# Optimization experiments

Hardware: AMD Instinct MI355X
Metric: run time of the kernel (lower is better)

The kernel has to match this reference:

```python
import jax, jax.numpy as jnp
import numpy as np

H = 512   # hidden_size
L = 20    # num_labels
B, S = 32, 256


def _uniform(key, shape, k):
    return jax.random.uniform(key, shape, minval=-k, maxval=k, dtype=jnp.float32)


def setup_inputs() -> dict:
    key = jax.random.key(0)
    ks = iter(jax.random.split(key, 40))
    k = 1.0 / np.sqrt(H)
    inp = {
        "inputs": jax.random.normal(next(ks), (B, S, H), dtype=jnp.float32),
        "labels": jax.random.randint(next(ks), (B, S), 0, L),
        "mask": jnp.ones((B, S), dtype=jnp.int32),
    }
    for layer, din in ((0, H), (1, 2 * H)):
        for d in ("f", "b"):
            inp[f"w_ih_l{layer}{d}"] = _uniform(next(ks), (4 * H, din), k)
            inp[f"w_hh_l{layer}{d}"] = _uniform(next(ks), (4 * H, H), k)
            inp[f"b_ih_l{layer}{d}"] = _uniform(next(ks), (4 * H,), k)
            inp[f"b_hh_l{layer}{d}"] = _uniform(next(ks), (4 * H,), k)
    kf = 1.0 / np.sqrt(2 * H)
    inp["fc_w"] = _uniform(next(ks), (L, 2 * H), kf)
    inp["fc_b"] = _uniform(next(ks), (L,), kf)
    inp["trans_m"] = jax.random.normal(next(ks), (L, L), dtype=jnp.float32) * 0.1
    inp["start_scores"] = jax.random.normal(next(ks), (L,), dtype=jnp.float32) * 0.1
    inp["end_scores"] = jax.random.normal(next(ks), (L,), dtype=jnp.float32) * 0.1
    return inp


def _lstm_dir(x, wih, whh, bih, bhh, reverse):
    # x: [S, B, Din] -> hs: [S, B, H] (outputs in original time order)
    _, b, _ = x.shape
    hh = whh.shape[1]
    xw = jnp.einsum('sbd,gd->sbg', x, wih) + bih + bhh  # precompute input projections

    def step(carry, xt):
        h, c = carry
        g = xt + h @ whh.T  # [B, 4H]
        i, f, gg, o = jnp.split(g, 4, axis=-1)  # pytorch gate order i,f,g,o
        c = jax.nn.sigmoid(f) * c + jax.nn.sigmoid(i) * jnp.tanh(gg)
        h = jax.nn.sigmoid(o) * jnp.tanh(c)
        return (h, c), h

    init = (jnp.zeros((b, hh), x.dtype), jnp.zeros((b, hh), x.dtype))
    _, hs = jax.lax.scan(step, init, xw, reverse=reverse)
    return hs


def _crf_loss(logits, tags, maskf, trans, start, end):
    # logits [S,B,L], tags [S,B], maskf [S,B] float. Returns per-sample NLL [B].
    s, b, n = logits.shape
    # --- normalizer (forward algorithm) ---
    alpha0 = logits[0] + start  # [B, n]

    def step(alpha, inp):
        emit, m = inp  # emit [B,n], m [B]
        tmp = alpha[:, :, None] + trans[None, :, :] + emit[:, None, :]  # [B, from, to]
        new = jax.nn.logsumexp(tmp, axis=1)
        alpha = jnp.where(m[:, None] > 0, new, alpha)
        return alpha, None

    alpha, _ = jax.lax.scan(step, alpha0, (logits[1:], maskf[1:]))
    norm = jax.nn.logsumexp(alpha + end, axis=1)  # [B]
    # --- gold path score ---
    emit = jnp.take_along_axis(logits, tags[:, :, None], axis=2)[:, :, 0] * maskf  # [S,B]
    trans_sc = trans[tags[:-1], tags[1:]] * maskf[1:]  # [S-1,B]
    last_idx = maskf.sum(0).astype(jnp.int32) - 1  # [B]
    last_tags = tags[last_idx, jnp.arange(b)]
    gold = emit.sum(0) + trans_sc.sum(0) + start[tags[0]] + end[last_tags]
    return norm - gold


def reference(inputs, labels, mask,
              w_ih_l0f, w_hh_l0f, b_ih_l0f, b_hh_l0f,
              w_ih_l0b, w_hh_l0b, b_ih_l0b, b_hh_l0b,
              w_ih_l1f, w_hh_l1f, b_ih_l1f, b_hh_l1f,
              w_ih_l1b, w_hh_l1b, b_ih_l1b, b_hh_l1b,
              fc_w, fc_b, trans_m, start_scores, end_scores):
    x = jnp.transpose(inputs, (1, 0, 2))  # [S,B,H]
    h0 = jnp.concatenate([
        _lstm_dir(x, w_ih_l0f, w_hh_l0f, b_ih_l0f, b_hh_l0f, False),
        _lstm_dir(x, w_ih_l0b, w_hh_l0b, b_ih_l0b, b_hh_l0b, True),
    ], axis=-1)  # [S,B,2H]
    h1 = jnp.concatenate([
        _lstm_dir(h0, w_ih_l1f, w_hh_l1f, b_ih_l1f, b_hh_l1f, False),
        _lstm_dir(h0, w_ih_l1b, w_hh_l1b, b_ih_l1b, b_hh_l1b, True),
    ], axis=-1)  # [S,B,2H]
    logits = h1 @ fc_w.T + fc_b  # [S,B,L]
    tags = labels.T  # [S,B]
    maskf = mask.T.astype(logits.dtype)
    loss = _crf_loss(logits, tags, maskf, trans_m, start_scores, end_scores)
    return loss.mean()
```

## Files before the change

### kernel.cpp

```cpp
#include <hip/hip_runtime.h>

#define Sx 256
#define Bx 32
#define Hx 512
#define Gx 2048
#define Lx 20
#define Rx 8192

typedef __attribute__((ext_vector_type(8))) short short8;
typedef __attribute__((ext_vector_type(4))) float f32x4;
typedef __attribute__((ext_vector_type(16))) float f32x16;

__device__ __forceinline__ unsigned short f2bf(float f) {
  union { float f; unsigned u; } v; v.f = f;
  unsigned u = v.u;
  return (unsigned short)((u + 0x7fffu + ((u >> 16) & 1u)) >> 16);
}
__device__ __forceinline__ float bf2f(unsigned short h) {
  union { unsigned u; float f; } v; v.u = ((unsigned)h) << 16;
  return v.f;
}
__device__ __forceinline__ float bfh(unsigned long long x, int r) {
  return bf2f((unsigned short)((x >> (16 * r)) & 0xffffull));
}

__device__ __forceinline__ float fsigm(float x) {
  return __builtin_amdgcn_rcpf(1.0f + __builtin_amdgcn_exp2f(-1.44269504f * x));
}
__device__ __forceinline__ float ftanh(float x) {
  return __builtin_fmaf(-2.0f,
      __builtin_amdgcn_rcpf(1.0f + __builtin_amdgcn_exp2f(2.88539008f * x)), 1.0f);
}
#define L2E 1.44269504088896f
#define LN2 0.69314718055995f

#define GLD16(gp, lp) __builtin_amdgcn_global_load_lds( \
    (const __attribute__((address_space(1))) void*)(gp), \
    (__attribute__((address_space(3))) void*)(lp), 16, 0, 0)


__global__ void k_pack_x(const float* __restrict__ x, unsigned short* __restrict__ xbf) {
  int tid = blockIdx.x * 256 + threadIdx.x;
  int h = tid & (Hx - 1);
  int r = tid >> 9;
  int b = r & 31;
  int t = r >> 5;
  xbf[tid] = f2bf(x[(b * Sx + t) * Hx + h]);
}

__global__ __launch_bounds__(256) void k_prep(
    const float* __restrict__ s0, const float* __restrict__ s1,
    const float* __restrict__ s2, const float* __restrict__ s3,
    const float* __restrict__ s4, const float* __restrict__ s5,
    const float* __restrict__ s6, const float* __restrict__ s7,
    unsigned short* __restrict__ d0, unsigned short* __restrict__ d1,
    unsigned short* __restrict__ d2, unsigned short* __restrict__ d3,
    unsigned short* __restrict__ d4, unsigned short* __restrict__ d5,
    unsigned short* __restrict__ d6, unsigned short* __restrict__ d7,
    const float* __restrict__ ba0, const float* __restrict__ bb0, float* __restrict__ bo0,
    const float* __restrict__ ba1, const float* __restrict__ bb1, float* __restrict__ bo1,
    const float* __restrict__ ba2, const float* __restrict__ bb2, float* __restrict__ bo2,
    const float* __restrict__ ba3, const float* __restrict__ bb3, float* __restrict__ bo3)
{
  const int blk = blockIdx.x;
  const int tid = threadIdx.x;
  if (blk < 5120) {
    const float* srcs[8] = { s0, s1, s2, s3, s4, s5, s6, s7 };
    unsigned short* dsts[8] = { d0, d1, d2, d3, d4, d5, d6, d7 };
    size_t e0 = ((size_t)blk * 256 + tid) * 8;
    int m = (int)(e0 >> 20);
    int seg; size_t base;
    if (m < 4)      { seg = m; base = (size_t)m << 20; }
    else if (m < 6) { seg = 4; base = (size_t)4 << 20; }
    else if (m < 8) { seg = 5; base = (size_t)6 << 20; }
    else if (m == 8){ seg = 6; base = (size_t)8 << 20; }
    else            { seg = 7; base = (size_t)9 << 20; }
    size_t off = e0 - base;
    f32x4 a = *(const f32x4*)(srcs[seg] + off);
    f32x4 b = *(const f32x4*)(srcs[seg] + off + 4);
    short8 o;
    o[0] = (short)f2bf(a[0]); o[1] = (short)f2bf(a[1]);
    o[2] = (short)f2bf(a[2]); o[3] = (short)f2bf(a[3]);
    o[4] = (short)f2bf(b[0]); o[5] = (short)f2bf(b[1]);
    o[6] = (short)f2bf(b[2]); o[7] = (short)f2bf(b[3]);
    *(short8*)(dsts[seg] + off) = o;
  } else {
    int j = blk - 5120;
    const float* bas[4] = { ba0, ba1, ba2, ba3 };
    const float* bbs[4] = { bb0, bb1, bb2, bb3 };
    float* bos[4] = { bo0, bo1, bo2, bo3 };
    int i0 = tid * 8;
    f32x4 x0 = *(const f32x4*)(bas[j] + i0);
    f32x4 x1 = *(const f32x4*)(bas[j] + i0 + 4);
    f32x4 y0 = *(const f32x4*)(bbs[j] + i0);
    f32x4 y1 = *(const f32x4*)(bbs[j] + i0 + 4);
    *(f32x4*)(bos[j] + i0) = x0 + y0;
    *(f32x4*)(bos[j] + i0 + 4) = x1 + y1;
  }
}

__global__ __launch_bounds__(256) void k_gemm(
    const unsigned short* __restrict__ A,
    const unsigned short* __restrict__ Bw,
    const float* __restrict__ bias,
    unsigned short* __restrict__ C,
    int M, int N, int K)
{
  const int bn = blockIdx.x, bm = blockIdx.y;
  const int tid = threadIdx.x;
  const int w = tid >> 6, lane = tid & 63;
  const int wr = w >> 1, wc = w & 1;
  const int lo = lane & 15, qd = lane >> 4;

  __shared__ unsigned short As[128 * 64];
  __shared__ unsigned short Bs[128 * 64];

  f32x4 acc[4][4] = {};

  const int cis = (lane & 7) ^ (lane >> 3);
  const int ktn = K >> 6;
  for (int kt = 0; kt < ktn; ++kt) {
    __syncthreads();
#pragma unroll
    for (int p = 0; p < 4; ++p) {
      int rowb = w * 8 + p * 32;
      int row = rowb + (lane >> 3);
      GLD16(&A[(size_t)(bm * 128 + row) * K + kt * 64 + cis * 8], &As[rowb * 64]);
      GLD16(&Bw[(size_t)(bn * 128 + row) * K + kt * 64 + cis * 8], &Bs[rowb * 64]);
    }
    __syncthreads();
#pragma unroll
    for (int kk = 0; kk < 2; ++kk) {
      short8 af[4], bfr[4];
#pragma unroll
      for (int mi = 0; mi < 4; ++mi)
        af[mi] = *(const short8*)&As[(wr * 64 + mi * 16 + lo) * 64
                                     + (((kk * 4 + qd) ^ (lo & 7)) * 8)];
#pragma unroll
      for (int ni = 0; ni < 4; ++ni)
        bfr[ni] = *(const short8*)&Bs[(wc * 64 + ni * 16 + lo) * 64
                                      + (((kk * 4 + qd) ^ (lo & 7)) * 8)];
#pragma unroll
      for (int mi = 0; mi < 4; ++mi)
#pragma unroll
        for (int ni = 0; ni < 4; ++ni)
          acc[mi][ni] = __builtin_amdgcn_mfma_f32_16x16x32_bf16(af[mi], bfr[ni], acc[mi][ni], 0, 0, 0);
    }
  }
#pragma unroll
  for (int mi = 0; mi < 4; ++mi) {
#pragma unroll
    for (int ni = 0; ni < 4; ++ni) {
      int n = bn * 128 + wc * 64 + ni * 16 + lo;
      float bv = bias[n];
      int wsb = (n >> 4) & 31, cg = n >> 9, jl = n & 15;
      size_t base = (size_t)wsb * (Rx * 64) + (size_t)cg * 16 + jl;
#pragma unroll
      for (int r = 0; r < 4; ++r) {
        int m = bm * 128 + wr * 64 + mi * 16 + qd * 4 + r;
        C[base + (size_t)m * 64] = f2bf(acc[mi][ni][r] + bv);
      }
    }
  }
}

__global__ __launch_bounds__(256) void k_gemm_t(
    const unsigned short* __restrict__ hT,
    const unsigned short* __restrict__ Bw,
    const float* __restrict__ bias,
    unsigned short* __restrict__ C,
    int M, int N, int K)
{
  const int bn = blockIdx.x, bm = blockIdx.y;
  const int tid = threadIdx.x;
  const int w = tid >> 6, lane = tid & 63;
  const int wr = w >> 1, wc = w & 1;
  const int lo = lane & 15, qd = lane >> 4;

  __shared__ unsigned short As[128 * 64];
  __shared__ unsigned short Bs[128 * 64];

  f32x4 acc[4][4] = {};

  const int cis = (lane & 7) ^ (lane >> 3);
  const int ktn = K >> 6;
  for (int kt = 0; kt < ktn; ++kt) {
    __syncthreads();
#pragma unroll
    for (int p = 0; p < 4; ++p) {
      int rowb = w * 8 + p * 32;
      int row = rowb + (lane >> 3);
      int grow = bm * 128 + row;
      int t = grow >> 5, b = grow & 31;
      int k = kt * 64 + cis * 8;
      int dirx = k >> 9, kk2 = k & 511;
      GLD16(&hT[(size_t)dirx * (Sx * 16384) + (size_t)t * 16384
                + (size_t)(kk2 >> 3) * 256 + b * 8], &As[rowb * 64]);
      GLD16(&Bw[(size_t)(bn * 128 + row) * K + kt * 64 + cis * 8], &Bs[rowb * 64]);
    }
    __syncthreads();
#pragma unroll
    for (int kk = 0; kk < 2; ++kk) {
      short8 af[4], bfr[4];
#pragma unroll
      for (int mi = 0; mi < 4; ++mi)
        af[mi] = *(const short8*)&As[(wr * 64 + mi * 16 + lo) * 64
                                     + (((kk * 4 + qd) ^ (lo & 7)) * 8)];
#pragma unroll
      for (int ni = 0; ni < 4; ++ni)
        bfr[ni] = *(const short8*)&Bs[(wc * 64 + ni * 16 + lo) * 64
                                      + (((kk * 4 + qd) ^ (lo & 7)) * 8)];
#pragma unroll
      for (int mi = 0; mi < 4; ++mi)
#pragma unroll
        for (int ni = 0; ni < 4; ++ni)
          acc[mi][ni] = __builtin_amdgcn_mfma_f32_16x16x32_bf16(af[mi], bfr[ni], acc[mi][ni], 0, 0, 0);
    }
  }
#pragma unroll
  for (int mi = 0; mi < 4; ++mi) {
#pragma unroll
    for (int ni = 0; ni < 4; ++ni) {
      int n = bn * 128 + wc * 64 + ni * 16 + lo;
      float bv = bias[n];
      int wsb = (n >> 4) & 31, cg = n >> 9, jl = n & 15;
      size_t base = (size_t)wsb * (Rx * 64) + (size_t)cg * 16 + jl;
#pragma unroll
      for (int r = 0; r < 4; ++r) {
        int m = bm * 128 + wr * 64 + mi * 16 + qd * 4 + r;
        C[base + (size_t)m * 64] = f2bf(acc[mi][ni][r] + bv);
      }
    }
  }
}

__global__ __launch_bounds__(256, 1) void k_lstm(
    const unsigned short* __restrict__ xwF,
    const unsigned short* __restrict__ xwB,
    const unsigned short* __restrict__ whF,
    const unsigned short* __restrict__ whB,
    unsigned short* __restrict__ hT,
    unsigned int* __restrict__ flags,
    unsigned int* __restrict__ done)
{
  const int wg = blockIdx.x;
  const int tid = threadIdx.x;

  __shared__ unsigned short Ws[64 * 512];

  if (wg >= 64) {
    asm volatile("s_setprio 0");
    float a = 1.0f + (float)tid, bm = 1.0000001f, cm = 1.0e-7f;
    for (;;) {
#pragma unroll 8
      for (int i = 0; i < 512; ++i) a = __builtin_fmaf(a, bm, cm);
      if (__hip_atomic_load(done, __ATOMIC_RELAXED, __HIP_MEMORY_SCOPE_AGENT) >= 64u) break;
    }
    if (a == 123.456789f) ((volatile float*)hT)[0] = a;
    return;
  }

  asm volatile("s_setprio 3");
  const int dir = wg >> 5;
  const int vs = wg & 31;
  const int j0 = vs * 16;
  const unsigned short* xw = (dir ? xwB : xwF) + (size_t)vs * (Rx * 64);
  const unsigned short* wh = dir ? whB : whF;
  unsigned short* hTd = hT + (size_t)dir * (Sx * 16384);
  unsigned int* fl = flags + dir * 32 * 32;

  {
    const int l6 = tid & 63;
#pragma unroll
    for (int i = 0; i < 16; ++i) {
      int rr = (tid >> 6) * 16 + i;
      int g = ((rr >> 4) << 9) + j0 + (rr & 15);
      int pc = l6 ^ (rr & 7);
      *(short8*)&Ws[rr * 512 + pc * 8] = *(const short8*)&wh[(size_t)g * Hx + l6 * 8];
    }
  }
  __syncthreads();
  if (tid >= 64) return;

  const int lane = tid;
  const int bn = lane & 31;
  const int q  = lane >> 5;

  float cst[2][4] = {};

  for (int s = 0; s < Sx; ++s) {
    const int t = dir ? (Sx - 1 - s) : s;

    const unsigned short* xwt = xw + ((size_t)t * 32 + bn) * 64 + q * 4;
    unsigned long long xg[4][2];
#pragma unroll
    for (int c = 0; c < 4; ++c)
#pragma unroll
      for (int jg = 0; jg < 2; ++jg)
        xg[c][jg] = *(const unsigned long long*)(xwt + c * 16 + jg * 8);
    __asm__ __volatile__("" ::: "memory");

    f32x16 acc0, acc1;

    if (s > 0) {
      const unsigned tgt = (unsigned)s;
      const int tp = dir ? (t + 1) : (t - 1);
      const unsigned short* hb = hTd + (size_t)tp * 16384 + lane * 8;

      short8 hreg[32];
      for (;;) {
        unsigned v = __hip_atomic_load(fl + (lane & 31) * 32,
                                       __ATOMIC_RELAXED, __HIP_MEMORY_SCOPE_AGENT);
#pragma unroll
        for (int ks = 0; ks < 32; ++ks)
          hreg[ks] = *(const short8*)(hb + ks * 512);
#pragma unroll
        for (int ks = 0; ks < 32; ++ks)
          asm volatile("" :: "v"(hreg[ks]));
        if (__all((int)(v >= tgt))) break;
        __asm__ __volatile__("" ::: "memory");
      }
      __builtin_amdgcn_sched_barrier(0);

      f32x16 a0 = {}, a1 = {}, b0 = {}, b1 = {};
#pragma unroll
      for (int ks = 0; ks < 32; ks += 2) {
        int lc0 = ks * 2 + q, lc1 = (ks + 1) * 2 + q;
        int pc0 = lc0 ^ (bn & 7), pc1 = lc1 ^ (bn & 7);
        short8 af00 = *(const short8*)&Ws[bn * 512 + pc0 * 8];
        short8 af10 = *(const short8*)&Ws[(32 + bn) * 512 + pc0 * 8];
        short8 af01 = *(const short8*)&Ws[bn * 512 + pc1 * 8];
        short8 af11 = *(const short8*)&Ws[(32 + bn) * 512 + pc1 * 8];
        a0 = __builtin_amdgcn_mfma_f32_32x32x16_bf16(af00, hreg[ks],     a0, 0, 0, 0);
        a1 = __builtin_amdgcn_mfma_f32_32x32x16_bf16(af10, hreg[ks],     a1, 0, 0, 0);
        b0 = __builtin_amdgcn_mfma_f32_32x32x16_bf16(af01, hreg[ks + 1], b0, 0, 0, 0);
        b1 = __builtin_amdgcn_mfma_f32_32x32x16_bf16(af11, hreg[ks + 1], b1, 0, 0, 0);
      }
      acc0 = a0 + b0;
      acc1 = a1 + b1;
    } else {
      acc0 = (f32x16){};
      acc1 = (f32x16){};
    }

#pragma unroll
    for (int jg = 0; jg < 2; ++jg) {
      unsigned long long hv = 0;
#pragma unroll
      for (int r = 0; r < 4; ++r) {
        float iv = acc0[jg * 4 + r]     + bfh(xg[0][jg], r);
        float fv = acc0[8 + jg * 4 + r] + bfh(xg[1][jg], r);
        float gv = acc1[jg * 4 + r]     + bfh(xg[2][jg], r);
        float ov = acc1[8 + jg * 4 + r] + bfh(xg[3][jg], r);
        float ct = fsigm(fv) * cst[jg][r] + fsigm(iv) * ftanh(gv);
        cst[jg][r] = ct;
        float hvf = fsigm(ov) * ftanh(ct);
        hv |= (unsigned long long)f2bf(hvf) << (16 * r);
      }
      unsigned short* hw = hTd + (size_t)t * 16384 + ((size_t)(vs * 2 + jg) * 32 + bn) * 8 + q * 4;
      __hip_atomic_store((unsigned long long*)hw, hv,
                         __ATOMIC_RELAXED, __HIP_MEMORY_SCOPE_AGENT);
    }

    __asm__ __volatile__("s_waitcnt vmcnt(0)" ::: "memory");
    if (lane == 0)
      __hip_atomic_store(fl + vs * 32, (unsigned)(s + 1),
                         __ATOMIC_RELAXED, __HIP_MEMORY_SCOPE_AGENT);
  }

  if (lane == 0)
    __hip_atomic_fetch_add(done, 1u, __ATOMIC_RELAXED, __HIP_MEMORY_SCOPE_AGENT);
}

__global__ __launch_bounds__(256) void k_fc(
    const unsigned short* __restrict__ h1T,
    const float* __restrict__ fcw,
    const float* __restrict__ fcb,
    float* __restrict__ logits)
{
  int row = blockIdx.x;
  int t = row >> 5, b = row & 31;
  int l = threadIdx.x & 31;
  int sl = threadIdx.x >> 5;
  __shared__ float red[8][32];
  float p = 0.f;
  if (l < Lx) {
#pragma unroll 4
    for (int kt = sl * 16; kt < sl * 16 + 16; ++kt) {
      int k = kt * 8;
      int dir = k >> 9, kk = k & 511;
      const unsigned short* hp = h1T + (size_t)dir * (Sx * 16384) + (size_t)t * 16384
                                 + ((size_t)(kk >> 3) * 32 + b) * 8;
      short8 hv = *(const short8*)hp;
      const float* wr = fcw + l * 1024 + k;
      f32x4 w0 = *(const f32x4*)wr;
      f32x4 w1 = *(const f32x4*)(wr + 4);
      p += bf2f((unsigned short)hv[0]) * w0[0] + bf2f((unsigned short)hv[1]) * w0[1]
         + bf2f((unsigned short)hv[2]) * w0[2] + bf2f((unsigned short)hv[3]) * w0[3]
         + bf2f((unsigned short)hv[4]) * w1[0] + bf2f((unsigned short)hv[5]) * w1[1]
         + bf2f((unsigned short)hv[6]) * w1[2] + bf2f((unsigned short)hv[7]) * w1[3];
    }
  }
  red[sl][l] = p;
  __syncthreads();
  if (threadIdx.x < Lx) {
    float s = fcb[threadIdx.x];
#pragma unroll
    for (int i = 0; i < 8; ++i) s += red[i][threadIdx.x];
    logits[(size_t)row * Lx + threadIdx.x] = s;
  }
}

__global__ __launch_bounds__(64) void k_crf(
    const float* __restrict__ logits,
    const int* __restrict__ labels,
    const int* __restrict__ mask,
    const float* __restrict__ trans,
    const float* __restrict__ startv,
    const float* __restrict__ endv,
    float* __restrict__ out)
{
  int b = blockIdx.x;
  int tid = threadIdx.x;
  __shared__ float tr[Lx * Lx];
  __shared__ float al[2][Lx];
  __shared__ float norm_s;
  for (int i = tid; i < Lx * Lx; i += 64) tr[i] = trans[i];
  if (tid < Lx) al[0][tid] = logits[b * Lx + tid] + startv[tid];
  __syncthreads();
  int cur = 0;
  float em = (tid < Lx) ? logits[((size_t)1 * Bx + b) * Lx + tid] : 0.f;
  int m = mask[b * Sx + 1];
  for (int t = 1; t < Sx; ++t) {
    float em_next = 0.f;
    int m_next = 0;
    if (t + 1 < Sx) {
      if (tid < Lx) em_next = logits[((size_t)(t + 1) * Bx + b) * Lx + tid];
      m_next = mask[b * Sx + t + 1];
    }
    if (tid < Lx) {
      int to = tid;
      float v[Lx];
      float mx = -1e30f;
#pragma unroll
      for (int f = 0; f < Lx; ++f) { v[f] = al[cur][f] + tr[f * Lx + to]; mx = fmaxf(mx, v[f]); }
      float sum = 0.f;
#pragma unroll
      for (int f = 0; f < Lx; ++f) sum += __builtin_amdgcn_exp2f((v[f] - mx) * L2E);
      float nv = mx + LN2 * __builtin_amdgcn_logf(sum) + em;
      al[1 - cur][to] = (m > 0) ? nv : al[cur][to];
    }
    __syncthreads();
    cur ^= 1;
    em = em_next;
    m = m_next;
  }
  if (tid == 0) {
    float mx = -1e30f;
    for (int l = 0; l < Lx; ++l) mx = fmaxf(mx, al[cur][l] + endv[l]);
    float s = 0.f;
    for (int l = 0; l < Lx; ++l) s += __builtin_amdgcn_exp2f((al[cur][l] + endv[l] - mx) * L2E);
    norm_s = mx + LN2 * __builtin_amdgcn_logf(s);
  }
  __syncthreads();
  const int* lab = labels + b * Sx;
  const int* msk = mask + b * Sx;
  float part = 0.f;
  int msum = 0;
  for (int t = tid; t < Sx; t += 64) {
    int mm = msk[t];
    int tg = lab[t];
    if (mm > 0) {
      part += logits[((size_t)t * Bx + b) * Lx + tg];
      if (t >= 1) part += tr[lab[t - 1] * Lx + tg];
      msum++;
    }
  }
#pragma unroll
  for (int o = 32; o > 0; o >>= 1) {
    part += __shfl_down(part, o, 64);
    msum += __shfl_down(msum, o, 64);
  }
  if (tid == 0) {
    float gold = part + startv[lab[0]] + endv[lab[msum - 1]];
    atomicAdd(out, (norm_s - gold) * (1.0f / 32.0f));
  }
}


extern "C" void kernel_launch(void* const* d_in, const int* in_sizes, int n_in,
                              void* d_out, int out_size, void* d_ws, size_t ws_size,
                              hipStream_t stream)
{
  const float* x      = (const float*)d_in[0];
  const int* labels   = (const int*)d_in[1];
  const int* mask     = (const int*)d_in[2];
  const float* wih0f  = (const float*)d_in[3];
  const float* whh0f  = (const float*)d_in[4];
  const float* bih0f  = (const float*)d_in[5];
  const float* bhh0f  = (const float*)d_in[6];
  const float* wih0b  = (const float*)d_in[7];
  const float* whh0b  = (const float*)d_in[8];
  const float* bih0b  = (const float*)d_in[9];
  const float* bhh0b  = (const float*)d_in[10];
  const float* wih1f  = (const float*)d_in[11];
  const float* whh1f  = (const float*)d_in[12];
  const float* bih1f  = (const float*)d_in[13];
  const float* bhh1f  = (const float*)d_in[14];
  const float* wih1b  = (const float*)d_in[15];
  const float* whh1b  = (const float*)d_in[16];
  const float* bih1b  = (const float*)d_in[17];
  const float* bhh1b  = (const float*)d_in[18];
  const float* fcw    = (const float*)d_in[19];
  const float* fcb    = (const float*)d_in[20];
  const float* transm = (const float*)d_in[21];
  const float* startv = (const float*)d_in[22];
  const float* endv   = (const float*)d_in[23];

  char* p = (char*)d_ws;
  auto alloc = [&](size_t bytes) -> char* {
    char* r = p;
    p += (bytes + 255) & ~((size_t)255);
    return r;
  };

  unsigned short* x_bf    = (unsigned short*)alloc((size_t)Rx * Hx * 2);
  unsigned short* wih0f_b = (unsigned short*)alloc((size_t)Gx * Hx * 2);
  unsigned short* wih0b_b = (unsigned short*)alloc((size_t)Gx * Hx * 2);
  unsigned short* whh0f_b = (unsigned short*)alloc((size_t)Gx * Hx * 2);
  unsigned short* whh0b_b = (unsigned short*)alloc((size_t)Gx * Hx * 2);
  unsigned short* wih1f_b = (unsigned short*)alloc((size_t)Gx * 1024 * 2);
  unsigned short* wih1b_b = (unsigned short*)alloc((size_t)Gx * 1024 * 2);
  unsigned short* whh1f_b = (unsigned short*)alloc((size_t)Gx * Hx * 2);
  unsigned short* whh1b_b = (unsigned short*)alloc((size_t)Gx * Hx * 2);
  float* bias0f = (float*)alloc(Gx * 4);
  float* bias0b = (float*)alloc(Gx * 4);
  float* bias1f = (float*)alloc(Gx * 4);
  float* bias1b = (float*)alloc(Gx * 4);
  unsigned short* xw_f = (unsigned short*)alloc((size_t)Rx * Gx * 2);
  unsigned short* xw_b = (unsigned short*)alloc((size_t)Rx * Gx * 2);
  unsigned short* h0T  = (unsigned short*)alloc((size_t)2 * Sx * 16384 * 2);
  unsigned short* h1T  = (unsigned short*)alloc((size_t)2 * Sx * 16384 * 2);
  float* logits = (float*)alloc((size_t)Rx * Lx * 4);
  unsigned int* flagsA = (unsigned int*)alloc(2 * 32 * 32 * 4);
  unsigned int* flagsB = (unsigned int*)alloc(2 * 32 * 32 * 4);
  unsigned int* doneA  = (unsigned int*)alloc(256);
  unsigned int* doneB  = (unsigned int*)alloc(256);

  if ((size_t)(p - (char*)d_ws) > ws_size) return;

  hipMemsetAsync(flagsA, 0, 2 * 32 * 32 * 4, stream);
  hipMemsetAsync(flagsB, 0, 2 * 32 * 32 * 4, stream);
  hipMemsetAsync(doneA, 0, 256, stream);
  hipMemsetAsync(doneB, 0, 256, stream);

  k_pack_x<<<(Rx * Hx) / 256, 256, 0, stream>>>(x, x_bf);
  k_prep<<<5124, 256, 0, stream>>>(
      wih0f, wih0b, whh0f, whh0b, wih1f, wih1b, whh1f, whh1b,
      wih0f_b, wih0b_b, whh0f_b, whh0b_b, wih1f_b, wih1b_b, whh1f_b, whh1b_b,
      bih0f, bhh0f, bias0f,
      bih0b, bhh0b, bias0b,
      bih1f, bhh1f, bias1f,
      bih1b, bhh1b, bias1b);

  k_gemm<<<dim3(Gx / 128, Rx / 128), 256, 0, stream>>>(x_bf, wih0f_b, bias0f, xw_f, Rx, Gx, Hx);
  k_gemm<<<dim3(Gx / 128, Rx / 128), 256, 0, stream>>>(x_bf, wih0b_b, bias0b, xw_b, Rx, Gx, Hx);
  k_lstm<<<256, 256, 0, stream>>>(xw_f, xw_b, whh0f_b, whh0b_b, h0T, flagsA, doneA);

  k_gemm_t<<<dim3(Gx / 128, Rx / 128), 256, 0, stream>>>(h0T, wih1f_b, bias1f, xw_f, Rx, Gx, 1024);
  k_gemm_t<<<dim3(Gx / 128, Rx / 128), 256, 0, stream>>>(h0T, wih1b_b, bias1b, xw_b, Rx, Gx, 1024);
  k_lstm<<<256, 256, 0, stream>>>(xw_f, xw_b, whh1f_b, whh1b_b, h1T, flagsB, doneB);

  k_fc<<<Rx, 256, 0, stream>>>(h1T, fcw, fcb, logits);
  hipMemsetAsync(d_out, 0, 4, stream);
  k_crf<<<Bx, 64, 0, stream>>>(logits, labels, mask, transm, startv, endv, (float*)d_out);
}
```

Measured before the change: 2.502 ms.

## Overlap layer-1 input projection GEMM with layer-0 LSTM recurrence using idle workgroups

Workgroups that previously only spun in the layer-0 LSTM kernel now pull GEMM tiles from an atomic work queue. Each tile waits on the per-direction timestep flags until the h0 rows it needs are ready, then computes the layer-1 input projection into new buffers. The goal is to hide the separate layer-1 GEMM launches behind the serial recurrence. Tiles are ordered from the middle outward so they become ready early for both directions. In exchange it adds two extra xw buffers and possible contention (memory bandwidth, flag polling) with the latency-critical recurrent workgroups.

```diff
diff --git a/kernel.cpp b/kernel.cpp
--- a/kernel.cpp
+++ b/kernel.cpp
@@ -164,76 +164,6 @@
   }
 }
 
-__global__ __launch_bounds__(256) void k_gemm_t(
-    const unsigned short* __restrict__ hT,
-    const unsigned short* __restrict__ Bw,
-    const float* __restrict__ bias,
-    unsigned short* __restrict__ C,
-    int M, int N, int K)
-{
-  const int bn = blockIdx.x, bm = blockIdx.y;
-  const int tid = threadIdx.x;
-  const int w = tid >> 6, lane = tid & 63;
-  const int wr = w >> 1, wc = w & 1;
-  const int lo = lane & 15, qd = lane >> 4;
-
-  __shared__ unsigned short As[128 * 64];
-  __shared__ unsigned short Bs[128 * 64];
-
-  f32x4 acc[4][4] = {};
-
-  const int cis = (lane & 7) ^ (lane >> 3);
-  const int ktn = K >> 6;
-  for (int kt = 0; kt < ktn; ++kt) {
-    __syncthreads();
-#pragma unroll
-    for (int p = 0; p < 4; ++p) {
-      int rowb = w * 8 + p * 32;
-      int row = rowb + (lane >> 3);
-      int grow = bm * 128 + row;
-      int t = grow >> 5, b = grow & 31;
-      int k = kt * 64 + cis * 8;
-      int dirx = k >> 9, kk2 = k & 511;
-      GLD16(&hT[(size_t)dirx * (Sx * 16384) + (size_t)t * 16384
-                + (size_t)(kk2 >> 3) * 256 + b * 8], &As[rowb * 64]);
-      GLD16(&Bw[(size_t)(bn * 128 + row) * K + kt * 64 + cis * 8], &Bs[rowb * 64]);
-    }
-    __syncthreads();
-#pragma unroll
-    for (int kk = 0; kk < 2; ++kk) {
-      short8 af[4], bfr[4];
-#pragma unroll
-      for (int mi = 0; mi < 4; ++mi)
-        af[mi] = *(const short8*)&As[(wr * 64 + mi * 16 + lo) * 64
-                                     + (((kk * 4 + qd) ^ (lo & 7)) * 8)];
-#pragma unroll
-      for (int ni = 0; ni < 4; ++ni)
-        bfr[ni] = *(const short8*)&Bs[(wc * 64 + ni * 16 + lo) * 64
-                                      + (((kk * 4 + qd) ^ (lo & 7)) * 8)];
-#pragma unroll
-      for (int mi = 0; mi < 4; ++mi)
-#pragma unroll
-        for (int ni = 0; ni < 4; ++ni)
-          acc[mi][ni] = __builtin_amdgcn_mfma_f32_16x16x32_bf16(af[mi], bfr[ni], acc[mi][ni], 0, 0, 0);
-    }
-  }
-#pragma unroll
-  for (int mi = 0; mi < 4; ++mi) {
-#pragma unroll
-    for (int ni = 0; ni < 4; ++ni) {
-      int n = bn * 128 + wc * 64 + ni * 16 + lo;
-      float bv = bias[n];
-      int wsb = (n >> 4) & 31, cg = n >> 9, jl = n & 15;
-      size_t base = (size_t)wsb * (Rx * 64) + (size_t)cg * 16 + jl;
-#pragma unroll
-      for (int r = 0; r < 4; ++r) {
-        int m = bm * 128 + wr * 64 + mi * 16 + qd * 4 + r;
-        C[base + (size_t)m * 64] = f2bf(acc[mi][ni][r] + bv);
-      }
-    }
-  }
-}
-
 __global__ __launch_bounds__(256, 1) void k_lstm(
     const unsigned short* __restrict__ xwF,
     const unsigned short* __restrict__ xwB,
@@ -241,22 +171,119 @@
     const unsigned short* __restrict__ whB,
     unsigned short* __restrict__ hT,
     unsigned int* __restrict__ flags,
-    unsigned int* __restrict__ done)
+    unsigned int* __restrict__ done,
+    const unsigned short* __restrict__ gWf,
+    const unsigned short* __restrict__ gWb,
+    const float* __restrict__ gBf,
+    const float* __restrict__ gBb,
+    unsigned short* __restrict__ gCf,
+    unsigned short* __restrict__ gCb,
+    unsigned int* __restrict__ wq,
+    int gw)
 {
   const int wg = blockIdx.x;
   const int tid = threadIdx.x;
 
   __shared__ unsigned short Ws[64 * 512];
+  __shared__ unsigned widx;
 
   if (wg >= 64) {
     asm volatile("s_setprio 0");
-    float a = 1.0f + (float)tid, bm = 1.0000001f, cm = 1.0e-7f;
-    for (;;) {
+    if (gw) {
+      const int w = tid >> 6, lane = tid & 63;
+      const int wr = w >> 1, wc = w & 1;
+      const int lo = lane & 15, qd = lane >> 4;
+      const int cis = (lane & 7) ^ (lane >> 3);
+      for (;;) {
+        if (tid == 0) widx = atomicAdd(wq, 1u);
+        __syncthreads();
+        unsigned idx = widx;
+        __syncthreads();
+        if (idx >= 2048u) break;
+        int r = (int)(idx >> 5), sub = (int)(idx & 31);
+        int dir1 = sub >> 4, bn = sub & 15;
+        int bm = (r & 1) ? (32 - ((r + 1) >> 1)) : (32 + (r >> 1));
+        unsigned tF = (unsigned)(4 * bm + 4), tB = (unsigned)(256 - 4 * bm);
+        if (tid < 64) {
+          for (;;) {
+            unsigned v = __hip_atomic_load(flags + (lane >> 5) * 1024 + (lane & 31) * 32,
+                                           __ATOMIC_RELAXED, __HIP_MEMORY_SCOPE_AGENT);
+            unsigned tgt = (lane < 32) ? tF : tB;
+            if (__all((int)(v >= tgt))) break;
+            if (__hip_atomic_load(done, __ATOMIC_RELAXED, __HIP_MEMORY_SCOPE_AGENT) >= 64u)
+              break;
+            float aa = 1.0f;
+#pragma unroll 4
+            for (int i = 0; i < 512; ++i) aa = __builtin_fmaf(aa, 1.0000001f, 1e-7f);
+            asm volatile("" :: "v"(aa));
+          }
+        }
+        __syncthreads();
+        const unsigned short* Bw = dir1 ? gWb : gWf;
+        const float* bias = dir1 ? gBb : gBf;
+        unsigned short* Cq = dir1 ? gCb : gCf;
+        f32x4 acc[4][4] = {};
+        for (int kt = 0; kt < 16; ++kt) {
+          __syncthreads();
+#pragma unroll
+          for (int p = 0; p < 4; ++p) {
+            int rowb = w * 8 + p * 32;
+            int row = rowb + (lane >> 3);
+            int grow = bm * 128 + row;
+            int t2 = grow >> 5, b2 = grow & 31;
+            int k = kt * 64 + cis * 8;
+            int dirx = k >> 9, kk2 = k & 511;
+            GLD16(&hT[(size_t)dirx * (Sx * 16384) + (size_t)t2 * 16384
+                      + (size_t)(kk2 >> 3) * 256 + b2 * 8], &Ws[rowb * 64]);
+            GLD16(&Bw[(size_t)(bn * 128 + row) * 1024 + kt * 64 + cis * 8],
+                  &Ws[8192 + rowb * 64]);
+          }
+          __syncthreads();
+#pragma unroll
+          for (int kk = 0; kk < 2; ++kk) {
+            short8 af[4], bfr[4];
+#pragma unroll
+            for (int mi = 0; mi < 4; ++mi)
+              af[mi] = *(const short8*)&Ws[(wr * 64 + mi * 16 + lo) * 64
+                                           + (((kk * 4 + qd) ^ (lo & 7)) * 8)];
+#pragma unroll
+            for (int ni = 0; ni < 4; ++ni)
+              bfr[ni] = *(const short8*)&Ws[8192 + (wc * 64 + ni * 16 + lo) * 64
+                                            + (((kk * 4 + qd) ^ (lo & 7)) * 8)];
+#pragma unroll
+            for (int mi = 0; mi < 4; ++mi)
+#pragma unroll
+              for (int ni = 0; ni < 4; ++ni)
+                acc[mi][ni] = __builtin_amdgcn_mfma_f32_16x16x32_bf16(af[mi], bfr[ni], acc[mi][ni], 0, 0, 0);
+          }
+        }
+#pragma unroll
+        for (int mi = 0; mi < 4; ++mi) {
+#pragma unroll
+          for (int ni = 0; ni < 4; ++ni) {
+            int n = bn * 128 + wc * 64 + ni * 16 + lo;
+            float bv = bias[n];
+            int wsb = (n >> 4) & 31, cg = n >> 9, jl = n & 15;
+            size_t base = (size_t)wsb * (Rx * 64) + (size_t)cg * 16 + jl;
+#pragma unroll
+            for (int r2 = 0; r2 < 4; ++r2) {
+              int m2 = bm * 128 + wr * 64 + mi * 16 + qd * 4 + r2;
+              Cq[base + (size_t)m2 * 64] = f2bf(acc[mi][ni][r2] + bv);
+            }
+          }
+        }
+        __syncthreads();
+      }
+    }
+    {
+      float a = 1.0f + (float)tid, bm2 = 1.0000001f, cm = 1.0e-7f;
+      for (;;) {
 #pragma unroll 8
-      for (int i = 0; i < 512; ++i) a = __builtin_fmaf(a, bm, cm);
-      if (__hip_atomic_load(done, __ATOMIC_RELAXED, __HIP_MEMORY_SCOPE_AGENT) >= 64u) break;
-    }
-    if (a == 123.456789f) ((volatile float*)hT)[0] = a;
+        for (int i = 0; i < 512; ++i) a = __builtin_fmaf(a, bm2, cm);
+        if (__hip_atomic_load(done, __ATOMIC_RELAXED, __HIP_MEMORY_SCOPE_AGENT) >= 64u) break;
+      }
+      if (a == 123.456789f) ((volatile float*)hT)[0] = a;
+    }
     return;
   }
 
@@ -537,8 +564,10 @@
   float* bias0b = (float*)alloc(Gx * 4);
   float* bias1f = (float*)alloc(Gx * 4);
   float* bias1b = (float*)alloc(Gx * 4);
-  unsigned short* xw_f = (unsigned short*)alloc((size_t)Rx * Gx * 2);
-  unsigned short* xw_b = (unsigned short*)alloc((size_t)Rx * Gx * 2);
+  unsigned short* xw_f  = (unsigned short*)alloc((size_t)Rx * Gx * 2);
+  unsigned short* xw_b  = (unsigned short*)alloc((size_t)Rx * Gx * 2);
+  unsigned short* xw1_f = (unsigned short*)alloc((size_t)Rx * Gx * 2);
+  unsigned short* xw1_b = (unsigned short*)alloc((size_t)Rx * Gx * 2);
   unsigned short* h0T  = (unsigned short*)alloc((size_t)2 * Sx * 16384 * 2);
   unsigned short* h1T  = (unsigned short*)alloc((size_t)2 * Sx * 16384 * 2);
   float* logits = (float*)alloc((size_t)Rx * Lx * 4);
@@ -546,6 +575,7 @@
   unsigned int* flagsB = (unsigned int*)alloc(2 * 32 * 32 * 4);
   unsigned int* doneA  = (unsigned int*)alloc(256);
   unsigned int* doneB  = (unsigned int*)alloc(256);
+  unsigned int* wq     = (unsigned int*)alloc(256);
 
   if ((size_t)(p - (char*)d_ws) > ws_size) return;
 
@@ -553,6 +583,7 @@
   hipMemsetAsync(flagsB, 0, 2 * 32 * 32 * 4, stream);
   hipMemsetAsync(doneA, 0, 256, stream);
   hipMemsetAsync(doneB, 0, 256, stream);
+  hipMemsetAsync(wq, 0, 256, stream);
 
   k_pack_x<<<(Rx * Hx) / 256, 256, 0, stream>>>(x, x_bf);
   k_prep<<<5124, 256, 0, stream>>>(
@@ -565,11 +596,15 @@
 
   k_gemm<<<dim3(Gx / 128, Rx / 128), 256, 0, stream>>>(x_bf, wih0f_b, bias0f, xw_f, Rx, Gx, Hx);
   k_gemm<<<dim3(Gx / 128, Rx / 128), 256, 0, stream>>>(x_bf, wih0b_b, bias0b, xw_b, Rx, Gx, Hx);
-  k_lstm<<<256, 256, 0, stream>>>(xw_f, xw_b, whh0f_b, whh0b_b, h0T, flagsA, doneA);
-
-  k_gemm_t<<<dim3(Gx / 128, Rx / 128), 256, 0, stream>>>(h0T, wih1f_b, bias1f, xw_f, Rx, Gx, 1024);
-  k_gemm_t<<<dim3(Gx / 128, Rx / 128), 256, 0, stream>>>(h0T, wih1b_b, bias1b, xw_b, Rx, Gx, 1024);
-  k_lstm<<<256, 256, 0, stream>>>(xw_f, xw_b, whh1f_b, whh1b_b, h1T, flagsB, doneB);
+
+  k_lstm<<<256, 256, 0, stream>>>(xw_f, xw_b, whh0f_b, whh0b_b, h0T, flagsA, doneA,
+                                  wih1f_b, wih1b_b, bias1f, bias1b, xw1_f, xw1_b, wq, 1);
+
+  k_lstm<<<256, 256, 0, stream>>>(xw1_f, xw1_b, whh1f_b, whh1b_b, h1T, flagsB, doneB,
+                                  (const unsigned short*)nullptr, (const unsigned short*)nullptr,
+                                  (const float*)nullptr, (const float*)nullptr,
+                                  (unsigned short*)nullptr, (unsigned short*)nullptr,
+                                  (unsigned int*)nullptr, 0);
 
   k_fc<<<Rx, 256, 0, stream>>>(h1T, fcw, fcb, logits);
   hipMemsetAsync(d_out, 0, 4, stream);
```

After: 2.429 ms (median of 2 runs). -2.9%, faster.
